# Optimization experiments

Measured on AMD Instinct MI355X. Metric: run time of the kernel, lower is better.

The kernel has to match this reference:

```python
import jax, jax.numpy as jnp
import numpy as np

C = 512
B, Q, H, W = 4, 4, 64, 64


def setup_inputs() -> dict:
    key = jax.random.key(0)
    ks = jax.random.split(key, 16)
    s = 1.0 / np.sqrt(C)
    sb = 1.0 / np.sqrt(C // 4)
    return {
        "x1": jax.random.normal(ks[0], (B, C, Q, H, W), jnp.float32),
        "x2": jax.random.normal(ks[1], (B, C, Q, H, W), jnp.float32),
        "Wq": jax.random.normal(ks[2], (C, C), jnp.float32) * s,
        "bq": jnp.zeros((C,), jnp.float32),
        "Wk": jax.random.normal(ks[3], (C, C), jnp.float32) * s,
        "bk": jnp.zeros((C,), jnp.float32),
        "Wv": jax.random.normal(ks[4], (C, C), jnp.float32) * s,
        "bv": jnp.zeros((C,), jnp.float32),
        "Wa1": jax.random.normal(ks[5], (C // 4, C), jnp.float32) * s,
        "ba1": jnp.zeros((C // 4,), jnp.float32),
        "Wa2": jax.random.normal(ks[6], (4, C // 4), jnp.float32) * sb,
        "ba2": jnp.zeros((4,), jnp.float32),
        "Wo": jax.random.normal(ks[7], (C, C), jnp.float32) * s,
        "bo": jnp.zeros((C,), jnp.float32),
        "gamma": jnp.ones((C,), jnp.float32),
        "beta": jnp.zeros((C,), jnp.float32),
    }


def _conv1x1(x, Wt, b):
    # shared 1x1 conv applied independently to each quaternion component
    # x: [B, Cin, Q, H, W] -> [B, Cout, Q, H, W]
    return jnp.einsum("oc,bcqhw->boqhw", Wt, x) + b[None, :, None, None, None]


def reference(x1, x2, Wq, bq, Wk, bk, Wv, bv, Wa1, ba1, Wa2, ba2, Wo, bo, gamma, beta):
    Bn, Cn, Qn, Hn, Wn = x1.shape
    G = Cn // 4  # head dim / channel groups
    q = _conv1x1(x1, Wq, bq)
    k = _conv1x1(x2, Wk, bk)
    v = _conv1x1(x2, Wv, bv)
    # angle gate: C -> C//4 -> relu -> 4, softmax over the 4 gate channels
    aw = jax.nn.softmax(_conv1x1(jax.nn.relu(_conv1x1(x1, Wa1, ba1)), Wa2, ba2), axis=1)  # [B,4,Q,H,W]
    def gate(t):
        return (t.reshape(Bn, G, 4, Qn, Hn, Wn) * aw[:, None]).reshape(Bn, Cn, Qn, Hn, Wn)
    q = gate(q)
    k = gate(k)
    S = Qn * Hn * Wn
    def heads(t):
        # [B,C,Q,H,W] -> [B, 4 heads, G, S]
        return t.reshape(Bn, G, 4, S).transpose(0, 2, 1, 3)
    qh, kh, vh = heads(q), heads(k), heads(v)
    scale = 1.0 / jnp.sqrt(jnp.asarray(G, qh.dtype))
    attn = jax.nn.softmax(jnp.einsum("bhgs,bhfs->bhgf", qh, kh) * scale, axis=-1)  # [B,4,G,G]
    out = jnp.einsum("bhgf,bhfs->bhgs", attn, vh)  # [B,4,G,S]
    out = out.transpose(0, 2, 1, 3).reshape(Bn, Cn, Qn, Hn, Wn)
    out = _conv1x1(out, Wo, bo)
    # IQBN: normalize each (channel, quaternion component) over (B,H,W)
    mean = out.mean(axis=(0, 3, 4), keepdims=True)
    var = out.var(axis=(0, 3, 4), keepdims=True)
    out = (out - mean) / jnp.sqrt(var + 1e-5)
    return out * gamma[None, :, None, None, None] + beta[None, :, None, None, None]
```

## Files before the change

### kernel.cpp

```cpp
#include <hip/hip_runtime.h>


#define DEVI __device__ __forceinline__
typedef unsigned short u16;
typedef __bf16 bf16x8 __attribute__((ext_vector_type(8)));
typedef float f32x4 __attribute__((ext_vector_type(4)));

DEVI float bf2f(unsigned int u) {
  union { unsigned int u; float f; } v; v.u = u << 16; return v.f;
}
DEVI u16 f2bf(float f) {
  union { float f; unsigned int u; } v; v.f = f;
  unsigned int r = v.u + 0x7FFFu + ((v.u >> 16) & 1u);
  return (u16)(r >> 16);
}
DEVI void gload_lds16(const void* gp, void* lp) {
  __builtin_amdgcn_global_load_lds((const __attribute__((address_space(1))) int*)gp,
                                   (__attribute__((address_space(3))) int*)lp, 16, 0, 0);
}

__global__ __launch_bounds__(256) void cvt_k(const float* __restrict__ in, u16* __restrict__ out, int n4) {
  int i = blockIdx.x * 256 + threadIdx.x;
  if (i < n4) {
    float4 v = reinterpret_cast<const float4*>(in)[i];
    ushort4 o; o.x = f2bf(v.x); o.y = f2bf(v.y); o.z = f2bf(v.z); o.w = f2bf(v.w);
    reinterpret_cast<ushort4*>(out)[i] = o;
  }
}

__global__ __launch_bounds__(256) void transpose_cvt(const float* __restrict__ in, u16* __restrict__ out,
                                                     int R, int Cc, long sIn, long sOut) {
  __shared__ float tile[64][65];
  const int t = threadIdx.x;
  const int c0 = blockIdx.x * 64, r0 = blockIdx.y * 64, b = blockIdx.z;
  const float* ip = in + (long)b * sIn;
  u16* op = out + (long)b * sOut;
#pragma unroll
  for (int i = 0; i < 4; ++i) {
    int r = (t >> 4) + i * 16;
    int c = (t & 15) * 4;
    float4 v = *reinterpret_cast<const float4*>(ip + (long)(r0 + r) * Cc + c0 + c);
    tile[r][c] = v.x; tile[r][c + 1] = v.y; tile[r][c + 2] = v.z; tile[r][c + 3] = v.w;
  }
  __syncthreads();
#pragma unroll
  for (int i = 0; i < 4; ++i) {
    int c = (t >> 4) + i * 16;
    int r = (t & 15) * 4;
    ushort4 o;
    o.x = f2bf(tile[r][c]); o.y = f2bf(tile[r + 1][c]);
    o.z = f2bf(tile[r + 2][c]); o.w = f2bf(tile[r + 3][c]);
    *reinterpret_cast<ushort4*>(op + (long)(c0 + c) * R + r0 + r) = o;
  }
}

__global__ __launch_bounds__(256) void woh_k(const float* __restrict__ Wo, u16* __restrict__ Woh) {
  int idx = blockIdx.x * 256 + threadIdx.x;
  int h = idx >> 16;
  int o = (idx >> 7) & 511;
  int g = idx & 127;
  union { float f; unsigned int u; } v; v.f = Wo[(long)o * 512 + 4 * g + h];
  unsigned int r = v.u + 0x7FFFu + ((v.u >> 16) & 1u);
  Woh[idx] = (u16)(r >> 16);
}

enum { MODE_GATE = 0, MODE_BIAS = 1, MODE_PLAIN = 2, MODE_FOLD1 = 3 };

template <int MODE>
__global__ __launch_bounds__(256) void gemm_bt(const u16* __restrict__ A, const u16* __restrict__ Bt,
                                               u16* __restrict__ C, const float* __restrict__ bias,
                                               const float* __restrict__ aw, int M, int N, int K,
                                               long sA, long sB, long sC) {
  __shared__ u16 As[128 * 64];
  __shared__ u16 Bs[128 * 64];
  const int t = threadIdx.x;
  const int bn = blockIdx.x, bm = blockIdx.y, bz = blockIdx.z;
  const u16* Ab;
  const u16* Bb;
  if constexpr (MODE == MODE_FOLD1) {
    Ab = A + (long)(bz & 3) * 512 * 128;
    Bb = Bt + (long)bz * 128 * 128;
  } else {
    Ab = A + (long)bz * sA;
    Bb = Bt + (long)bz * sB;
  }
  const u16* Atile = Ab + (long)(bm * 128) * K;
  const u16* Btile = Bb + (long)(bn * 128) * K;
  const int wid = t >> 6, l = t & 63;
  const int rbase = (wid >> 1) * 64, cbase = (wid & 1) * 64;
  const int lr = l & 15, lkb = (l >> 4) * 8, hi = l >> 4;
  f32x4 acc[4][4] = {};
  for (int kt = 0; kt < K; kt += 64) {
#pragma unroll
    for (int i = 0; i < 4; ++i) {
      int idx = t + i * 256;
      int r = idx >> 3, cc = (idx & 7) * 8;
      gload_lds16(Atile + (long)r * K + kt + cc, &As[idx * 8]);
      gload_lds16(Btile + (long)r * K + kt + cc, &Bs[idx * 8]);
    }
    __syncthreads();
#pragma unroll
    for (int s = 0; s < 2; ++s) {
      bf16x8 av[4], bv[4];
#pragma unroll
      for (int m = 0; m < 4; ++m)
        av[m] = *reinterpret_cast<const bf16x8*>(&As[(rbase + m * 16 + lr) * 64 + s * 32 + lkb]);
#pragma unroll
      for (int n = 0; n < 4; ++n)
        bv[n] = *reinterpret_cast<const bf16x8*>(&Bs[(cbase + n * 16 + lr) * 64 + s * 32 + lkb]);
#pragma unroll
      for (int m = 0; m < 4; ++m)
#pragma unroll
        for (int n = 0; n < 4; ++n)
          acc[m][n] = __builtin_amdgcn_mfma_f32_16x16x32_bf16(av[m], bv[n], acc[m][n], 0, 0, 0);
    }
    __syncthreads();
  }
#pragma unroll
  for (int m = 0; m < 4; ++m) {
#pragma unroll
    for (int r = 0; r < 4; ++r) {
      int row = bm * 128 + rbase + m * 16 + hi * 4 + r;
      float bval = 0.f;
      if constexpr (MODE == MODE_GATE) bval = bias[row];
      if constexpr (MODE == MODE_BIAS) bval = bias[bz * M + row];
#pragma unroll
      for (int n = 0; n < 4; ++n) {
        int col = bn * 128 + cbase + n * 16 + lr;
        float v = acc[m][n][r] + bval;
        if constexpr (MODE == MODE_GATE)
          v *= aw[((long)bz * 4 + (row & 3)) * N + col];
        if constexpr (MODE == MODE_FOLD1)
          C[((long)(bz >> 2) * 512 + row) * 512 + 4 * col + (bz & 3)] = f2bf(v);
        else
          C[(long)bz * sC + (long)row * N + col] = f2bf(v);
      }
    }
  }
}

__global__ __launch_bounds__(256) void gemm_a1_aw(const u16* __restrict__ Wa1b, const u16* __restrict__ X1t,
                                                  const float* __restrict__ ba1, const float* __restrict__ Wa2,
                                                  const float* __restrict__ ba2, float* __restrict__ AW) {
  __shared__ union {
    struct { u16 As[128 * 64]; u16 Bs[128 * 64]; } st;
    float a1s[128][129];
  } u;
  __shared__ float wa2s[512];
  const int t = threadIdx.x;
  const int bn = blockIdx.x, bz = blockIdx.z;
  for (int i = t; i < 512; i += 256) wa2s[i] = Wa2[i];
  const u16* Btile = X1t + (long)bz * 16384 * 512 + (long)(bn * 128) * 512;
  const int wid = t >> 6, l = t & 63;
  const int rbase = (wid >> 1) * 64, cbase = (wid & 1) * 64;
  const int lr = l & 15, lkb = (l >> 4) * 8, hi = l >> 4;
  f32x4 acc[4][4] = {};
  for (int kt = 0; kt < 512; kt += 64) {
#pragma unroll
    for (int i = 0; i < 4; ++i) {
      int idx = t + i * 256;
      int r = idx >> 3, cc = (idx & 7) * 8;
      gload_lds16(Wa1b + (long)r * 512 + kt + cc, &u.st.As[idx * 8]);
      gload_lds16(Btile + (long)r * 512 + kt + cc, &u.st.Bs[idx * 8]);
    }
    __syncthreads();
#pragma unroll
    for (int s = 0; s < 2; ++s) {
      bf16x8 av[4], bv[4];
#pragma unroll
      for (int m = 0; m < 4; ++m)
        av[m] = *reinterpret_cast<const bf16x8*>(&u.st.As[(rbase + m * 16 + lr) * 64 + s * 32 + lkb]);
#pragma unroll
      for (int n = 0; n < 4; ++n)
        bv[n] = *reinterpret_cast<const bf16x8*>(&u.st.Bs[(cbase + n * 16 + lr) * 64 + s * 32 + lkb]);
#pragma unroll
      for (int m = 0; m < 4; ++m)
#pragma unroll
        for (int n = 0; n < 4; ++n)
          acc[m][n] = __builtin_amdgcn_mfma_f32_16x16x32_bf16(av[m], bv[n], acc[m][n], 0, 0, 0);
    }
    __syncthreads();
  }
#pragma unroll
  for (int m = 0; m < 4; ++m) {
#pragma unroll
    for (int r = 0; r < 4; ++r) {
      int row = rbase + m * 16 + hi * 4 + r;
      float bval = ba1[row];
#pragma unroll
      for (int n = 0; n < 4; ++n) {
        int col = cbase + n * 16 + lr;
        float v = acc[m][n][r] + bval;
        u.a1s[col][row] = v > 0.f ? v : 0.f;
      }
    }
  }
  __syncthreads();
  if (t < 128) {
    float a0 = ba2[0], a1 = ba2[1], a2 = ba2[2], a3 = ba2[3];
#pragma unroll 4
    for (int c = 0; c < 128; ++c) {
      float av = u.a1s[t][c];
      a0 += wa2s[c] * av; a1 += wa2s[128 + c] * av;
      a2 += wa2s[256 + c] * av; a3 += wa2s[384 + c] * av;
    }
    float mx = fmaxf(fmaxf(a0, a1), fmaxf(a2, a3));
    float e0 = __expf(a0 - mx), e1 = __expf(a1 - mx), e2 = __expf(a2 - mx), e3 = __expf(a3 - mx);
    float inv = 1.f / (e0 + e1 + e2 + e3);
    long sg = (long)bn * 128 + t;
    float* awp = AW + (long)bz * 4 * 16384;
    awp[sg] = e0 * inv;
    awp[16384 + sg] = e1 * inv;
    awp[2 * 16384 + sg] = e2 * inv;
    awp[3 * 16384 + sg] = e3 * inv;
  }
}

__global__ __launch_bounds__(256) void logits_k(const u16* __restrict__ Q, const u16* __restrict__ Kt,
                                                float* __restrict__ L) {
  __shared__ u16 As[128 * 64];
  __shared__ u16 Bs[128 * 64];
  const int S = 16384;
  const int ks = blockIdx.x;
  const int bh = blockIdx.y;
  const int b = bh >> 2, h = bh & 3;
  const int t = threadIdx.x;
  const int wid = t >> 6, l = t & 63;
  const int rbase = (wid >> 1) * 64, cbase = (wid & 1) * 64;
  const int lr = l & 15, lkb = (l >> 4) * 8, hi = l >> 4;
  const u16* qb = Q + (long)b * 512 * S + (long)h * S;
  const u16* kb = Kt + (long)b * 512 * S + (long)h * S;
  const int k0 = ks * 2048;
  f32x4 acc[4][4] = {};
  for (int kt = 0; kt < 2048; kt += 64) {
    int kk = k0 + kt;
#pragma unroll
    for (int i = 0; i < 4; ++i) {
      int idx = t + i * 256;
      int r = idx >> 3, cc = (idx & 7) * 8;
      gload_lds16(qb + (long)4 * r * S + kk + cc, &As[idx * 8]);
      gload_lds16(kb + (long)4 * r * S + kk + cc, &Bs[idx * 8]);
    }
    __syncthreads();
#pragma unroll
    for (int s = 0; s < 2; ++s) {
      bf16x8 av[4], bv[4];
#pragma unroll
      for (int m = 0; m < 4; ++m)
        av[m] = *reinterpret_cast<const bf16x8*>(&As[(rbase + m * 16 + lr) * 64 + s * 32 + lkb]);
#pragma unroll
      for (int n = 0; n < 4; ++n)
        bv[n] = *reinterpret_cast<const bf16x8*>(&Bs[(cbase + n * 16 + lr) * 64 + s * 32 + lkb]);
#pragma unroll
      for (int m = 0; m < 4; ++m)
#pragma unroll
        for (int n = 0; n < 4; ++n)
          acc[m][n] = __builtin_amdgcn_mfma_f32_16x16x32_bf16(av[m], bv[n], acc[m][n], 0, 0, 0);
    }
    __syncthreads();
  }
  float* Lb = L + (long)bh * 128 * 128;
#pragma unroll
  for (int m = 0; m < 4; ++m)
#pragma unroll
    for (int r = 0; r < 4; ++r) {
      int row = rbase + m * 16 + hi * 4 + r;
#pragma unroll
      for (int n = 0; n < 4; ++n) {
        int col = cbase + n * 16 + lr;
        atomicAdd(&Lb[row * 128 + col], acc[m][n][r]);
      }
    }
}

__global__ __launch_bounds__(256) void softmax_attnT(const float* __restrict__ L, u16* __restrict__ attnT) {
  const float scale = 0.08838834764831845f;
  int row = blockIdx.x * 4 + (threadIdx.x >> 6);
  int l = threadIdx.x & 63;
  const float* p = L + (long)row * 128;
  float v0 = p[l] * scale, v1 = p[l + 64] * scale;
  float m = fmaxf(v0, v1);
  for (int off = 32; off; off >>= 1) m = fmaxf(m, __shfl_xor(m, off));
  float e0 = __expf(v0 - m), e1 = __expf(v1 - m);
  float s = e0 + e1;
  for (int off = 32; off; off >>= 1) s += __shfl_xor(s, off);
  float inv = 1.f / s;
  int bh = row >> 7, g = row & 127;
  u16* at = attnT + (long)bh * 16384 + g;
  at[(long)l * 128] = f2bf(e0 * inv);
  at[(long)(l + 64) * 128] = f2bf(e1 * inv);
}

__global__ __launch_bounds__(256) void b2_k(const u16* __restrict__ Weff, const float* __restrict__ bv,
                                            const float* __restrict__ bo, float* __restrict__ b2) {
  int idx = blockIdx.x * 256 + threadIdx.x;
  int b = idx >> 9, o = idx & 511;
  const u16* w = Weff + ((long)b * 512 + o) * 512;
  float s = bo[o];
  for (int c = 0; c < 512; ++c) s += bf2f(w[c]) * bv[c];
  b2[idx] = s;
}

__global__ __launch_bounds__(256) void stats_k(const u16* __restrict__ o2, float* __restrict__ stat) {
  const int g0 = blockIdx.x;
  const int c = g0 >> 2, qq = g0 & 3;
  const int t = threadIdx.x;
  float s1 = 0.f, s2 = 0.f;
#pragma unroll
  for (int b = 0; b < 4; ++b) {
    const u16* p = o2 + ((long)(b * 512 + c) * 16384) + qq * 4096;
#pragma unroll
    for (int j = 0; j < 2; ++j) {
      uint4 v = *reinterpret_cast<const uint4*>(p + (t + j * 256) * 8);
      const unsigned int* pv = reinterpret_cast<const unsigned int*>(&v);
#pragma unroll
      for (int e = 0; e < 4; ++e) {
        float f0 = bf2f(pv[e] & 0xffffu);
        float f1 = bf2f(pv[e] >> 16);
        s1 += f0 + f1;
        s2 += f0 * f0 + f1 * f1;
      }
    }
  }
  for (int off = 32; off; off >>= 1) { s1 += __shfl_xor(s1, off); s2 += __shfl_xor(s2, off); }
  __shared__ float r1[4], r2[4];
  if ((t & 63) == 0) { r1[t >> 6] = s1; r2[t >> 6] = s2; }
  __syncthreads();
  if (t == 0) {
    float S1 = r1[0] + r1[1] + r1[2] + r1[3];
    float S2 = r2[0] + r2[1] + r2[2] + r2[3];
    float mean = S1 * (1.f / 16384.f);
    float var = S2 * (1.f / 16384.f) - mean * mean;
    stat[g0 * 2] = mean;
    stat[g0 * 2 + 1] = 1.f / sqrtf(var + 1e-5f);
  }
}

__global__ __launch_bounds__(256) void norm_k(const u16* __restrict__ o2, const float* __restrict__ stat,
                                              const float* __restrict__ gamma, const float* __restrict__ beta,
                                              float* __restrict__ out) {
  long i8 = ((long)blockIdx.x * 256 + threadIdx.x) * 8;
  int c = (int)((i8 >> 14) & 511);
  int s = (int)(i8 & 16383);
  int g0 = c * 4 + (s >> 12);
  float mean = stat[g0 * 2], inv = stat[g0 * 2 + 1];
  float sc = inv * gamma[c];
  float sh = beta[c] - mean * sc;
  uint4 v = *reinterpret_cast<const uint4*>(o2 + i8);
  const unsigned int* pv = reinterpret_cast<const unsigned int*>(&v);
  float4 ra, rb;
  ra.x = bf2f(pv[0] & 0xffffu) * sc + sh; ra.y = bf2f(pv[0] >> 16) * sc + sh;
  ra.z = bf2f(pv[1] & 0xffffu) * sc + sh; ra.w = bf2f(pv[1] >> 16) * sc + sh;
  rb.x = bf2f(pv[2] & 0xffffu) * sc + sh; rb.y = bf2f(pv[2] >> 16) * sc + sh;
  rb.z = bf2f(pv[3] & 0xffffu) * sc + sh; rb.w = bf2f(pv[3] >> 16) * sc + sh;
  *reinterpret_cast<float4*>(out + i8) = ra;
  *reinterpret_cast<float4*>(out + i8 + 4) = rb;
}

extern "C" void kernel_launch(void* const* d_in, const int* in_sizes, int n_in,
                              void* d_out, int out_size, void* d_ws, size_t ws_size,
                              hipStream_t stream) {
  const float* x1 = (const float*)d_in[0];
  const float* x2 = (const float*)d_in[1];
  const float* Wq = (const float*)d_in[2];
  const float* bq = (const float*)d_in[3];
  const float* Wk = (const float*)d_in[4];
  const float* bk = (const float*)d_in[5];
  const float* Wv = (const float*)d_in[6];
  const float* bv = (const float*)d_in[7];
  const float* Wa1 = (const float*)d_in[8];
  const float* ba1 = (const float*)d_in[9];
  const float* Wa2 = (const float*)d_in[10];
  const float* ba2 = (const float*)d_in[11];
  const float* Wo = (const float*)d_in[12];
  const float* bo = (const float*)d_in[13];
  const float* gamma = (const float*)d_in[14];
  const float* beta = (const float*)d_in[15];
  float* out = (float*)d_out;

  char* ws = (char*)d_ws;
  const long MB = 1024L * 1024L;
  u16* X1T = (u16*)(ws);
  u16* X2T = (u16*)(ws + 64 * MB);
  u16* Qb  = (u16*)(ws + 128 * MB);
  u16* Kb  = (u16*)(ws + 192 * MB);
  float* AW = (float*)(ws + 256 * MB);
  float* L  = (float*)(ws + 257 * MB);
  u16* ATT  = (u16*)(ws + 258 * MB);
  u16* WEFF = (u16*)(ws + 259 * MB);
  u16* W2   = (u16*)(ws + 261 * MB);
  u16* WQB  = (u16*)(ws + 263 * MB);
  u16* WKB  = (u16*)(ws + 263 * MB + 512 * 1024);
  u16* WA1B = (u16*)(ws + 264 * MB);
  u16* WVT  = (u16*)(ws + 264 * MB + 256 * 1024);
  u16* WOH  = (u16*)(ws + 264 * MB + 768 * 1024);
  float* B2 = (float*)(ws + 265 * MB + 256 * 1024);
  float* STAT = (float*)(ws + 265 * MB + 512 * 1024);
  u16* O2 = X1T;
  (void)ws_size; (void)in_sizes; (void)n_in; (void)out_size;

  dim3 blk(256);
  const long SC = (long)16384 * 512;

  cvt_k<<<dim3(256), blk, 0, stream>>>(Wq, WQB, 65536);
  cvt_k<<<dim3(256), blk, 0, stream>>>(Wk, WKB, 65536);
  cvt_k<<<dim3(64), blk, 0, stream>>>(Wa1, WA1B, 16384);
  transpose_cvt<<<dim3(256, 8, 4), blk, 0, stream>>>(x1, X1T, 512, 16384, SC, SC);
  transpose_cvt<<<dim3(256, 8, 4), blk, 0, stream>>>(x2, X2T, 512, 16384, SC, SC);
  transpose_cvt<<<dim3(8, 8, 1), blk, 0, stream>>>(Wv, WVT, 512, 512, 0, 0);
  woh_k<<<dim3(1024), blk, 0, stream>>>(Wo, WOH);

  gemm_a1_aw<<<dim3(128, 1, 4), blk, 0, stream>>>(WA1B, X1T, ba1, Wa2, ba2, AW);

  gemm_bt<MODE_GATE><<<dim3(128, 4, 4), blk, 0, stream>>>(WQB, X1T, Qb, bq, AW, 512, 16384, 512, 0L, SC, SC);
  gemm_bt<MODE_GATE><<<dim3(128, 4, 4), blk, 0, stream>>>(WKB, X2T, Kb, bk, AW, 512, 16384, 512, 0L, SC, SC);

  hipMemsetAsync(L, 0, 16 * 128 * 128 * sizeof(float), stream);
  logits_k<<<dim3(8, 16), blk, 0, stream>>>(Qb, Kb, L);
  softmax_attnT<<<dim3(512), blk, 0, stream>>>(L, ATT);

  gemm_bt<MODE_FOLD1><<<dim3(1, 4, 16), blk, 0, stream>>>(WOH, ATT, WEFF, nullptr, nullptr, 512, 128, 128, 0L, 0L, 0L);
  b2_k<<<dim3(8), blk, 0, stream>>>(WEFF, bv, bo, B2);
  gemm_bt<MODE_PLAIN><<<dim3(4, 4, 4), blk, 0, stream>>>(WEFF, WVT, W2, nullptr, nullptr, 512, 512, 512,
                                                         512L * 512L, 0L, 512L * 512L);

  gemm_bt<MODE_BIAS><<<dim3(128, 4, 4), blk, 0, stream>>>(W2, X2T, O2, B2, nullptr, 512, 16384, 512,
                                                          512L * 512L, SC, SC);

  stats_k<<<dim3(2048), blk, 0, stream>>>(O2, STAT);
  norm_k<<<dim3(16384), blk, 0, stream>>>(O2, STAT, gamma, beta, out);
}
```

Measured before the change: 760.9 us.

## Double-buffer and swizzle GEMM tiles, head-major Q/K, split-K logits, fuse stats into GEMM

Several changes at once. All MFMA GEMMs get double-buffered LDS tiles with an XOR swizzle, so the next K-tile is prefetched while the current one is computed and LDS bank conflicts drop. Q/K are written head-major so logits read contiguous rows, and logits use a 32-way split-K into partial buffers summed in softmax instead of global atomics. BN statistics are accumulated in the final GEMM epilogue via LDS and global atomics, which removes the separate stats pass, and the weight conversions are merged into one kernel. The cost is more LDS per block, float atomics with nondeterministic ordering, and a single-pass variance (E[x^2]-mean^2) that is less numerically stable.

```diff
diff --git a/kernel.cpp b/kernel.cpp
--- a/kernel.cpp
+++ b/kernel.cpp
@@ -19,13 +19,17 @@
                                    (__attribute__((address_space(3))) int*)lp, 16, 0, 0);
 }
 
-__global__ __launch_bounds__(256) void cvt_k(const float* __restrict__ in, u16* __restrict__ out, int n4) {
+__global__ __launch_bounds__(256) void cvtW_k(const float* __restrict__ Wq, const float* __restrict__ Wk,
+                                              const float* __restrict__ Wa1, u16* __restrict__ WQB,
+                                              u16* __restrict__ WKB, u16* __restrict__ WA1B) {
   int i = blockIdx.x * 256 + threadIdx.x;
-  if (i < n4) {
-    float4 v = reinterpret_cast<const float4*>(in)[i];
-    ushort4 o; o.x = f2bf(v.x); o.y = f2bf(v.y); o.z = f2bf(v.z); o.w = f2bf(v.w);
-    reinterpret_cast<ushort4*>(out)[i] = o;
-  }
+  const float* src; u16* dst; int off;
+  if (i < 65536) { src = Wq; dst = WQB; off = i; }
+  else if (i < 131072) { src = Wk; dst = WKB; off = i - 65536; }
+  else { src = Wa1; dst = WA1B; off = i - 131072; }
+  float4 v = reinterpret_cast<const float4*>(src)[off];
+  ushort4 o; o.x = f2bf(v.x); o.y = f2bf(v.y); o.z = f2bf(v.z); o.w = f2bf(v.w);
+  reinterpret_cast<ushort4*>(dst)[off] = o;
 }
 
 __global__ __launch_bounds__(256) void transpose_cvt(const float* __restrict__ in, u16* __restrict__ out,
@@ -67,16 +71,16 @@
 enum { MODE_GATE = 0, MODE_BIAS = 1, MODE_PLAIN = 2, MODE_FOLD1 = 3 };
 
 template <int MODE>
-__global__ __launch_bounds__(256) void gemm_bt(const u16* __restrict__ A, const u16* __restrict__ Bt,
-                                               u16* __restrict__ C, const float* __restrict__ bias,
-                                               const float* __restrict__ aw, int M, int N, int K,
-                                               long sA, long sB, long sC) {
-  __shared__ u16 As[128 * 64];
-  __shared__ u16 Bs[128 * 64];
+__global__ __launch_bounds__(256, 2) void gemm_bt(const u16* __restrict__ A, const u16* __restrict__ Bt,
+                                                  u16* __restrict__ C, const float* __restrict__ bias,
+                                                  const float* __restrict__ aw, float* __restrict__ stata,
+                                                  int M, int N, int K, long sA, long sB, long sC) {
+  __shared__ u16 As[2][128 * 64];
+  __shared__ u16 Bs[2][128 * 64];
+  __shared__ float racc[128][2];
   const int t = threadIdx.x;
   const int bn = blockIdx.x, bm = blockIdx.y, bz = blockIdx.z;
-  const u16* Ab;
-  const u16* Bb;
+  const u16* Ab; const u16* Bb;
   if constexpr (MODE == MODE_FOLD1) {
     Ab = A + (long)(bz & 3) * 512 * 128;
     Bb = Bt + (long)bz * 128 * 128;
@@ -88,26 +92,45 @@
   const u16* Btile = Bb + (long)(bn * 128) * K;
   const int wid = t >> 6, l = t & 63;
   const int rbase = (wid >> 1) * 64, cbase = (wid & 1) * 64;
-  const int lr = l & 15, lkb = (l >> 4) * 8, hi = l >> 4;
+  const int lr = l & 15, hi = l >> 4;
   f32x4 acc[4][4] = {};
-  for (int kt = 0; kt < K; kt += 64) {
-#pragma unroll
-    for (int i = 0; i < 4; ++i) {
-      int idx = t + i * 256;
-      int r = idx >> 3, cc = (idx & 7) * 8;
-      gload_lds16(Atile + (long)r * K + kt + cc, &As[idx * 8]);
-      gload_lds16(Btile + (long)r * K + kt + cc, &Bs[idx * 8]);
-    }
-    __syncthreads();
+  const int nt = K >> 6;
+
+#pragma unroll
+  for (int i = 0; i < 4; ++i) {
+    int idx = t + i * 256;
+    int r = idx >> 3;
+    int gs = ((idx & 7) ^ (r & 7)) * 8;
+    gload_lds16(Atile + (long)r * K + gs, &As[0][idx * 8]);
+    gload_lds16(Btile + (long)r * K + gs, &Bs[0][idx * 8]);
+  }
+  __syncthreads();
+  int cur = 0;
+  for (int kt = 0; kt < nt; ++kt) {
+    if (kt + 1 < nt) {
+      int koff = (kt + 1) << 6;
+#pragma unroll
+      for (int i = 0; i < 4; ++i) {
+        int idx = t + i * 256;
+        int r = idx >> 3;
+        int gs = ((idx & 7) ^ (r & 7)) * 8;
+        gload_lds16(Atile + (long)r * K + koff + gs, &As[cur ^ 1][idx * 8]);
+        gload_lds16(Btile + (long)r * K + koff + gs, &Bs[cur ^ 1][idx * 8]);
+      }
+    }
 #pragma unroll
     for (int s = 0; s < 2; ++s) {
       bf16x8 av[4], bv[4];
 #pragma unroll
-      for (int m = 0; m < 4; ++m)
-        av[m] = *reinterpret_cast<const bf16x8*>(&As[(rbase + m * 16 + lr) * 64 + s * 32 + lkb]);
-#pragma unroll
-      for (int n = 0; n < 4; ++n)
-        bv[n] = *reinterpret_cast<const bf16x8*>(&Bs[(cbase + n * 16 + lr) * 64 + s * 32 + lkb]);
+      for (int m = 0; m < 4; ++m) {
+        int ra = rbase + m * 16 + lr;
+        av[m] = *reinterpret_cast<const bf16x8*>(&As[cur][ra * 64 + ((4 * s + hi) ^ (ra & 7)) * 8]);
+      }
+#pragma unroll
+      for (int n = 0; n < 4; ++n) {
+        int rb = cbase + n * 16 + lr;
+        bv[n] = *reinterpret_cast<const bf16x8*>(&Bs[cur][rb * 64 + ((4 * s + hi) ^ (rb & 7)) * 8]);
+      }
 #pragma unroll
       for (int m = 0; m < 4; ++m)
 #pragma unroll
@@ -115,35 +138,60 @@
           acc[m][n] = __builtin_amdgcn_mfma_f32_16x16x32_bf16(av[m], bv[n], acc[m][n], 0, 0, 0);
     }
     __syncthreads();
+    cur ^= 1;
+  }
+
+  int qq = 0;
+  if constexpr (MODE == MODE_BIAS) {
+    if (t < 128) { racc[t][0] = 0.f; racc[t][1] = 0.f; }
+    __syncthreads();
+    qq = bn >> 5;
   }
 #pragma unroll
   for (int m = 0; m < 4; ++m) {
 #pragma unroll
     for (int r = 0; r < 4; ++r) {
-      int row = bm * 128 + rbase + m * 16 + hi * 4 + r;
+      int rloc = rbase + m * 16 + hi * 4 + r;
+      int row = bm * 128 + rloc;
       float bval = 0.f;
       if constexpr (MODE == MODE_GATE) bval = bias[row];
       if constexpr (MODE == MODE_BIAS) bval = bias[bz * M + row];
+      float rs = 0.f, rq = 0.f;
 #pragma unroll
       for (int n = 0; n < 4; ++n) {
         int col = bn * 128 + cbase + n * 16 + lr;
         float v = acc[m][n][r] + bval;
-        if constexpr (MODE == MODE_GATE)
+        if constexpr (MODE == MODE_GATE) {
           v *= aw[((long)bz * 4 + (row & 3)) * N + col];
-        if constexpr (MODE == MODE_FOLD1)
+          C[((long)(bz * 4 + (row & 3)) * 128 + (row >> 2)) * 16384 + col] = f2bf(v);
+        } else if constexpr (MODE == MODE_FOLD1) {
           C[((long)(bz >> 2) * 512 + row) * 512 + 4 * col + (bz & 3)] = f2bf(v);
-        else
+        } else {
           C[(long)bz * sC + (long)row * N + col] = f2bf(v);
-      }
-    }
-  }
-}
-
-__global__ __launch_bounds__(256) void gemm_a1_aw(const u16* __restrict__ Wa1b, const u16* __restrict__ X1t,
-                                                  const float* __restrict__ ba1, const float* __restrict__ Wa2,
-                                                  const float* __restrict__ ba2, float* __restrict__ AW) {
+        }
+        if constexpr (MODE == MODE_BIAS) { rs += v; rq += v * v; }
+      }
+      if constexpr (MODE == MODE_BIAS) {
+        atomicAdd(&racc[rloc][0], rs);
+        atomicAdd(&racc[rloc][1], rq);
+      }
+    }
+  }
+  if constexpr (MODE == MODE_BIAS) {
+    __syncthreads();
+    if (t < 128) {
+      int c = bm * 128 + t;
+      atomicAdd(&stata[(c * 4 + qq) * 2], racc[t][0]);
+      atomicAdd(&stata[(c * 4 + qq) * 2 + 1], racc[t][1]);
+    }
+  }
+}
+
+__global__ __launch_bounds__(256, 2) void gemm_a1_aw(const u16* __restrict__ Wa1b, const u16* __restrict__ X1t,
+                                                     const float* __restrict__ ba1, const float* __restrict__ Wa2,
+                                                     const float* __restrict__ ba2, float* __restrict__ AW) {
   __shared__ union {
-    struct { u16 As[128 * 64]; u16 Bs[128 * 64]; } st;
+    struct { u16 As[2][128 * 64]; u16 Bs[2][128 * 64]; } st;
     float a1s[128][129];
   } u;
   __shared__ float wa2s[512];
@@ -153,26 +201,43 @@
   const u16* Btile = X1t + (long)bz * 16384 * 512 + (long)(bn * 128) * 512;
   const int wid = t >> 6, l = t & 63;
   const int rbase = (wid >> 1) * 64, cbase = (wid & 1) * 64;
-  const int lr = l & 15, lkb = (l >> 4) * 8, hi = l >> 4;
+  const int lr = l & 15, hi = l >> 4;
   f32x4 acc[4][4] = {};
-  for (int kt = 0; kt < 512; kt += 64) {
-#pragma unroll
-    for (int i = 0; i < 4; ++i) {
-      int idx = t + i * 256;
-      int r = idx >> 3, cc = (idx & 7) * 8;
-      gload_lds16(Wa1b + (long)r * 512 + kt + cc, &u.st.As[idx * 8]);
-      gload_lds16(Btile + (long)r * 512 + kt + cc, &u.st.Bs[idx * 8]);
-    }
-    __syncthreads();
+#pragma unroll
+  for (int i = 0; i < 4; ++i) {
+    int idx = t + i * 256;
+    int r = idx >> 3;
+    int gs = ((idx & 7) ^ (r & 7)) * 8;
+    gload_lds16(Wa1b + (long)r * 512 + gs, &u.st.As[0][idx * 8]);
+    gload_lds16(Btile + (long)r * 512 + gs, &u.st.Bs[0][idx * 8]);
+  }
+  __syncthreads();
+  int cur = 0;
+  for (int kt = 0; kt < 8; ++kt) {
+    if (kt < 7) {
+      int koff = (kt + 1) << 6;
+#pragma unroll
+      for (int i = 0; i < 4; ++i) {
+        int idx = t + i * 256;
+        int r = idx >> 3;
+        int gs = ((idx & 7) ^ (r & 7)) * 8;
+        gload_lds16(Wa1b + (long)r * 512 + koff + gs, &u.st.As[cur ^ 1][idx * 8]);
+        gload_lds16(Btile + (long)r * 512 + koff + gs, &u.st.Bs[cur ^ 1][idx * 8]);
+      }
+    }
 #pragma unroll
     for (int s = 0; s < 2; ++s) {
       bf16x8 av[4], bv[4];
 #pragma unroll
-      for (int m = 0; m < 4; ++m)
-        av[m] = *reinterpret_cast<const bf16x8*>(&u.st.As[(rbase + m * 16 + lr) * 64 + s * 32 + lkb]);
-#pragma unroll
-      for (int n = 0; n < 4; ++n)
-        bv[n] = *reinterpret_cast<const bf16x8*>(&u.st.Bs[(cbase + n * 16 + lr) * 64 + s * 32 + lkb]);
+      for (int m = 0; m < 4; ++m) {
+        int ra = rbase + m * 16 + lr;
+        av[m] = *reinterpret_cast<const bf16x8*>(&u.st.As[cur][ra * 64 + ((4 * s + hi) ^ (ra & 7)) * 8]);
+      }
+#pragma unroll
+      for (int n = 0; n < 4; ++n) {
+        int rb = cbase + n * 16 + lr;
+        bv[n] = *reinterpret_cast<const bf16x8*>(&u.st.Bs[cur][rb * 64 + ((4 * s + hi) ^ (rb & 7)) * 8]);
+      }
 #pragma unroll
       for (int m = 0; m < 4; ++m)
 #pragma unroll
@@ -180,6 +245,7 @@
           acc[m][n] = __builtin_amdgcn_mfma_f32_16x16x32_bf16(av[m], bv[n], acc[m][n], 0, 0, 0);
     }
     __syncthreads();
+    cur ^= 1;
   }
 #pragma unroll
   for (int m = 0; m < 4; ++m) {
@@ -216,41 +282,55 @@
   }
 }
 
-__global__ __launch_bounds__(256) void logits_k(const u16* __restrict__ Q, const u16* __restrict__ Kt,
-                                                float* __restrict__ L) {
-  __shared__ u16 As[128 * 64];
-  __shared__ u16 Bs[128 * 64];
-  const int S = 16384;
+__global__ __launch_bounds__(256, 2) void logits_k(const u16* __restrict__ Qh, const u16* __restrict__ Kh,
+                                                   float* __restrict__ Lp) {
+  __shared__ u16 As[2][128 * 64];
+  __shared__ u16 Bs[2][128 * 64];
+  const long S = 16384;
   const int ks = blockIdx.x;
   const int bh = blockIdx.y;
-  const int b = bh >> 2, h = bh & 3;
   const int t = threadIdx.x;
   const int wid = t >> 6, l = t & 63;
   const int rbase = (wid >> 1) * 64, cbase = (wid & 1) * 64;
-  const int lr = l & 15, lkb = (l >> 4) * 8, hi = l >> 4;
-  const u16* qb = Q + (long)b * 512 * S + (long)h * S;
-  const u16* kb = Kt + (long)b * 512 * S + (long)h * S;
-  const int k0 = ks * 2048;
+  const int lr = l & 15, hi = l >> 4;
+  const u16* qb = Qh + (long)bh * 128 * S + ks * 512;
+  const u16* kb = Kh + (long)bh * 128 * S + ks * 512;
   f32x4 acc[4][4] = {};
-  for (int kt = 0; kt < 2048; kt += 64) {
-    int kk = k0 + kt;
-#pragma unroll
-    for (int i = 0; i < 4; ++i) {
-      int idx = t + i * 256;
-      int r = idx >> 3, cc = (idx & 7) * 8;
-      gload_lds16(qb + (long)4 * r * S + kk + cc, &As[idx * 8]);
-      gload_lds16(kb + (long)4 * r * S + kk + cc, &Bs[idx * 8]);
-    }
-    __syncthreads();
+#pragma unroll
+  for (int i = 0; i < 4; ++i) {
+    int idx = t + i * 256;
+    int r = idx >> 3;
+    int gs = ((idx & 7) ^ (r & 7)) * 8;
+    gload_lds16(qb + (long)r * S + gs, &As[0][idx * 8]);
+    gload_lds16(kb + (long)r * S + gs, &Bs[0][idx * 8]);
+  }
+  __syncthreads();
+  int cur = 0;
+  for (int kt = 0; kt < 8; ++kt) {
+    if (kt < 7) {
+      int koff = (kt + 1) << 6;
+#pragma unroll
+      for (int i = 0; i < 4; ++i) {
+        int idx = t + i * 256;
+        int r = idx >> 3;
+        int gs = ((idx & 7) ^ (r & 7)) * 8;
+        gload_lds16(qb + (long)r * S + koff + gs, &As[cur ^ 1][idx * 8]);
+        gload_lds16(kb + (long)r * S + koff + gs, &Bs[cur ^ 1][idx * 8]);
+      }
+    }
 #pragma unroll
     for (int s = 0; s < 2; ++s) {
       bf16x8 av[4], bv[4];
 #pragma unroll
-      for (int m = 0; m < 4; ++m)
-        av[m] = *reinterpret_cast<const bf16x8*>(&As[(rbase + m * 16 + lr) * 64 + s * 32 + lkb]);
-#pragma unroll
-      for (int n = 0; n < 4; ++n)
-        bv[n] = *reinterpret_cast<const bf16x8*>(&Bs[(cbase + n * 16 + lr) * 64 + s * 32 + lkb]);
+      for (int m = 0; m < 4; ++m) {
+        int ra = rbase + m * 16 + lr;
+        av[m] = *reinterpret_cast<const bf16x8*>(&As[cur][ra * 64 + ((4 * s + hi) ^ (ra & 7)) * 8]);
+      }
+#pragma unroll
+      for (int n = 0; n < 4; ++n) {
+        int rb = cbase + n * 16 + lr;
+        bv[n] = *reinterpret_cast<const bf16x8*>(&Bs[cur][rb * 64 + ((4 * s + hi) ^ (rb & 7)) * 8]);
+      }
 #pragma unroll
       for (int m = 0; m < 4; ++m)
 #pragma unroll
@@ -258,8 +338,9 @@
           acc[m][n] = __builtin_amdgcn_mfma_f32_16x16x32_bf16(av[m], bv[n], acc[m][n], 0, 0, 0);
     }
     __syncthreads();
-  }
-  float* Lb = L + (long)bh * 128 * 128;
+    cur ^= 1;
+  }
+  float* Lb = Lp + ((long)ks * 16 + bh) * 16384;
 #pragma unroll
   for (int m = 0; m < 4; ++m)
 #pragma unroll
@@ -268,24 +349,30 @@
 #pragma unroll
       for (int n = 0; n < 4; ++n) {
         int col = cbase + n * 16 + lr;
-        atomicAdd(&Lb[row * 128 + col], acc[m][n][r]);
-      }
-    }
-}
-
-__global__ __launch_bounds__(256) void softmax_attnT(const float* __restrict__ L, u16* __restrict__ attnT) {
+        Lb[row * 128 + col] = acc[m][n][r];
+      }
+    }
+}
+
+__global__ __launch_bounds__(256) void softmax_attnT(const float* __restrict__ Lp, u16* __restrict__ attnT) {
   const float scale = 0.08838834764831845f;
   int row = blockIdx.x * 4 + (threadIdx.x >> 6);
   int l = threadIdx.x & 63;
-  const float* p = L + (long)row * 128;
-  float v0 = p[l] * scale, v1 = p[l + 64] * scale;
+  int bh = row >> 7, g = row & 127;
+  const float* base = Lp + (long)bh * 16384 + (long)g * 128;
+  float v0 = 0.f, v1 = 0.f;
+#pragma unroll 4
+  for (int sp = 0; sp < 32; ++sp) {
+    v0 += base[(long)sp * 16 * 16384 + l];
+    v1 += base[(long)sp * 16 * 16384 + l + 64];
+  }
+  v0 *= scale; v1 *= scale;
   float m = fmaxf(v0, v1);
   for (int off = 32; off; off >>= 1) m = fmaxf(m, __shfl_xor(m, off));
   float e0 = __expf(v0 - m), e1 = __expf(v1 - m);
   float s = e0 + e1;
   for (int off = 32; off; off >>= 1) s += __shfl_xor(s, off);
   float inv = 1.f / s;
-  int bh = row >> 7, g = row & 127;
   u16* at = attnT + (long)bh * 16384 + g;
   at[(long)l * 128] = f2bf(e0 * inv);
   at[(long)(l + 64) * 128] = f2bf(e1 * inv);
@@ -301,49 +388,17 @@
   b2[idx] = s;
 }
 
-__global__ __launch_bounds__(256) void stats_k(const u16* __restrict__ o2, float* __restrict__ stat) {
-  const int g0 = blockIdx.x;
-  const int c = g0 >> 2, qq = g0 & 3;
-  const int t = threadIdx.x;
-  float s1 = 0.f, s2 = 0.f;
-#pragma unroll
-  for (int b = 0; b < 4; ++b) {
-    const u16* p = o2 + ((long)(b * 512 + c) * 16384) + qq * 4096;
-#pragma unroll
-    for (int j = 0; j < 2; ++j) {
-      uint4 v = *reinterpret_cast<const uint4*>(p + (t + j * 256) * 8);
-      const unsigned int* pv = reinterpret_cast<const unsigned int*>(&v);
-#pragma unroll
-      for (int e = 0; e < 4; ++e) {
-        float f0 = bf2f(pv[e] & 0xffffu);
-        float f1 = bf2f(pv[e] >> 16);
-        s1 += f0 + f1;
-        s2 += f0 * f0 + f1 * f1;
-      }
-    }
-  }
-  for (int off = 32; off; off >>= 1) { s1 += __shfl_xor(s1, off); s2 += __shfl_xor(s2, off); }
-  __shared__ float r1[4], r2[4];
-  if ((t & 63) == 0) { r1[t >> 6] = s1; r2[t >> 6] = s2; }
-  __syncthreads();
-  if (t == 0) {
-    float S1 = r1[0] + r1[1] + r1[2] + r1[3];
-    float S2 = r2[0] + r2[1] + r2[2] + r2[3];
-    float mean = S1 * (1.f / 16384.f);
-    float var = S2 * (1.f / 16384.f) - mean * mean;
-    stat[g0 * 2] = mean;
-    stat[g0 * 2 + 1] = 1.f / sqrtf(var + 1e-5f);
-  }
-}
-
-__global__ __launch_bounds__(256) void norm_k(const u16* __restrict__ o2, const float* __restrict__ stat,
+__global__ __launch_bounds__(256) void norm_k(const u16* __restrict__ o2, const float* __restrict__ stata,
                                               const float* __restrict__ gamma, const float* __restrict__ beta,
                                               float* __restrict__ out) {
   long i8 = ((long)blockIdx.x * 256 + threadIdx.x) * 8;
   int c = (int)((i8 >> 14) & 511);
   int s = (int)(i8 & 16383);
   int g0 = c * 4 + (s >> 12);
-  float mean = stat[g0 * 2], inv = stat[g0 * 2 + 1];
+  float sum = stata[g0 * 2], sq = stata[g0 * 2 + 1];
+  float mean = sum * (1.f / 16384.f);
+  float var = sq * (1.f / 16384.f) - mean * mean;
+  float inv = rsqrtf(var + 1e-5f);
   float sc = inv * gamma[c];
   float sh = beta[c] - mean * sc;
   uint4 v = *reinterpret_cast<const uint4*>(o2 + i8);
@@ -382,10 +437,10 @@
   const long MB = 1024L * 1024L;
   u16* X1T = (u16*)(ws);
   u16* X2T = (u16*)(ws + 64 * MB);
-  u16* Qb  = (u16*)(ws + 128 * MB);
-  u16* Kb  = (u16*)(ws + 192 * MB);
+  u16* Qh  = (u16*)(ws + 128 * MB);
+  u16* Kh  = (u16*)(ws + 192 * MB);
   float* AW = (float*)(ws + 256 * MB);
-  float* L  = (float*)(ws + 257 * MB);
+  float* STATA = (float*)(ws + 257 * MB);
   u16* ATT  = (u16*)(ws + 258 * MB);
   u16* WEFF = (u16*)(ws + 259 * MB);
   u16* W2   = (u16*)(ws + 261 * MB);
@@ -395,38 +450,38 @@
   u16* WVT  = (u16*)(ws + 264 * MB + 256 * 1024);
   u16* WOH  = (u16*)(ws + 264 * MB + 768 * 1024);
   float* B2 = (float*)(ws + 265 * MB + 256 * 1024);
-  float* STAT = (float*)(ws + 265 * MB + 512 * 1024);
+  float* Lp = (float*)(ws);
   u16* O2 = X1T;
   (void)ws_size; (void)in_sizes; (void)n_in; (void)out_size;
 
   dim3 blk(256);
   const long SC = (long)16384 * 512;
 
-  cvt_k<<<dim3(256), blk, 0, stream>>>(Wq, WQB, 65536);
-  cvt_k<<<dim3(256), blk, 0, stream>>>(Wk, WKB, 65536);
-  cvt_k<<<dim3(64), blk, 0, stream>>>(Wa1, WA1B, 16384);
+  cvtW_k<<<dim3(576), blk, 0, stream>>>(Wq, Wk, Wa1, WQB, WKB, WA1B);
+  woh_k<<<dim3(1024), blk, 0, stream>>>(Wo, WOH);
+  transpose_cvt<<<dim3(8, 8, 1), blk, 0, stream>>>(Wv, WVT, 512, 512, 0, 0);
   transpose_cvt<<<dim3(256, 8, 4), blk, 0, stream>>>(x1, X1T, 512, 16384, SC, SC);
   transpose_cvt<<<dim3(256, 8, 4), blk, 0, stream>>>(x2, X2T, 512, 16384, SC, SC);
-  transpose_cvt<<<dim3(8, 8, 1), blk, 0, stream>>>(Wv, WVT, 512, 512, 0, 0);
-  woh_k<<<dim3(1024), blk, 0, stream>>>(Wo, WOH);
+  hipMemsetAsync(STATA, 0, 2048 * 2 * sizeof(float), stream);
 
   gemm_a1_aw<<<dim3(128, 1, 4), blk, 0, stream>>>(WA1B, X1T, ba1, Wa2, ba2, AW);
 
-  gemm_bt<MODE_GATE><<<dim3(128, 4, 4), blk, 0, stream>>>(WQB, X1T, Qb, bq, AW, 512, 16384, 512, 0L, SC, SC);
-  gemm_bt<MODE_GATE><<<dim3(128, 4, 4), blk, 0, stream>>>(WKB, X2T, Kb, bk, AW, 512, 16384, 512, 0L, SC, SC);
-
-  hipMemsetAsync(L, 0, 16 * 128 * 128 * sizeof(float), stream);
-  logits_k<<<dim3(8, 16), blk, 0, stream>>>(Qb, Kb, L);
-  softmax_attnT<<<dim3(512), blk, 0, stream>>>(L, ATT);
-
-  gemm_bt<MODE_FOLD1><<<dim3(1, 4, 16), blk, 0, stream>>>(WOH, ATT, WEFF, nullptr, nullptr, 512, 128, 128, 0L, 0L, 0L);
+  gemm_bt<MODE_GATE><<<dim3(128, 4, 4), blk, 0, stream>>>(WQB, X1T, Qh, bq, AW, nullptr,
+                                                          512, 16384, 512, 0L, SC, SC);
+  gemm_bt<MODE_GATE><<<dim3(128, 4, 4), blk, 0, stream>>>(WKB, X2T, Kh, bk, AW, nullptr,
+                                                          512, 16384, 512, 0L, SC, SC);
+
+  logits_k<<<dim3(32, 16), blk, 0, stream>>>(Qh, Kh, Lp);
+  softmax_attnT<<<dim3(512), blk, 0, stream>>>(Lp, ATT);
+
+  gemm_bt<MODE_FOLD1><<<dim3(1, 4, 16), blk, 0, stream>>>(WOH, ATT, WEFF, nullptr, nullptr, nullptr,
+                                                          512, 128, 128, 0L, 0L, 0L);
   b2_k<<<dim3(8), blk, 0, stream>>>(WEFF, bv, bo, B2);
-  gemm_bt<MODE_PLAIN><<<dim3(4, 4, 4), blk, 0, stream>>>(WEFF, WVT, W2, nullptr, nullptr, 512, 512, 512,
-                                                         512L * 512L, 0L, 512L * 512L);
-
-  gemm_bt<MODE_BIAS><<<dim3(128, 4, 4), blk, 0, stream>>>(W2, X2T, O2, B2, nullptr, 512, 16384, 512,
-                                                          512L * 512L, SC, SC);
-
-  stats_k<<<dim3(2048), blk, 0, stream>>>(O2, STAT);
-  norm_k<<<dim3(16384), blk, 0, stream>>>(O2, STAT, gamma, beta, out);
-}
+  gemm_bt<MODE_PLAIN><<<dim3(4, 4, 4), blk, 0, stream>>>(WEFF, WVT, W2, nullptr, nullptr, nullptr,
+                                                         512, 512, 512, 512L * 512L, 0L, 512L * 512L);
+
+  gemm_bt<MODE_BIAS><<<dim3(128, 4, 4), blk, 0, stream>>>(W2, X2T, O2, B2, nullptr, STATA,
+                                                          512, 16384, 512, 512L * 512L, SC, SC);
+
+  norm_k<<<dim3(16384), blk, 0, stream>>>(O2, STATA, gamma, beta, out);
+}
```

Measured after the change: 762.1 us. About the same (+0.2%).
